# Kernel optimization log

Hardware: AMD Instinct MI355X
Metric: run time of the kernel (lower is better)

Reference implementation:

```python
import jax, jax.numpy as jnp
import numpy as np

B, S, D = 32, 1024, 1024
H = 16            # attention heads
T = 8             # num_tasks (probe tokens)
E = 8             # num_experts
K = 2             # top_k
HID = 4 * D       # expert hidden dim
EPS = 1e-5


def setup_inputs() -> dict:
    key = jax.random.key(0)
    ks = jax.random.split(key, 12)
    sd = 1.0 / np.sqrt(D)
    inp = {
        "x": jax.random.normal(ks[0], (B, S, D), jnp.float32),
        "probe": jax.random.normal(ks[1], (1, T, D), jnp.float32) * 0.02,
        "in_proj_w": jax.random.normal(ks[2], (3 * D, D), jnp.float32) * sd,
        "in_proj_b": jnp.zeros((3 * D,), jnp.float32),
        "out_proj_w": jax.random.normal(ks[3], (D, D), jnp.float32) * sd,
        "out_proj_b": jnp.zeros((D,), jnp.float32),
        "ln_gamma": jnp.ones((D,), jnp.float32),
        "ln_beta": jnp.zeros((D,), jnp.float32),
        "gate_w": jax.random.normal(ks[4], (T, D, E), jnp.float32) * sd,  # per-task gate (task-aware)
        "w1": jax.random.normal(ks[5], (E, D, HID), jnp.float32) * sd,
        "b1": jnp.zeros((E, HID), jnp.float32),
        "w2": jax.random.normal(ks[6], (E, HID, D), jnp.float32) / np.sqrt(HID),
        "b2": jnp.zeros((E, D), jnp.float32),
    }
    return inp


def reference(x, probe, in_proj_w, in_proj_b, out_proj_w, out_proj_b,
              ln_gamma, ln_beta, gate_w, w1, b1, w2, b2):
    b, s, d = x.shape
    t = probe.shape[1]
    dh = d // H
    # --- multihead cross attention: query = probe, key/value = x ---
    wq, wk, wv = in_proj_w[:d], in_proj_w[d:2 * d], in_proj_w[2 * d:]
    bq, bk, bv = in_proj_b[:d], in_proj_b[d:2 * d], in_proj_b[2 * d:]
    q = jnp.broadcast_to(probe, (b, t, d)) @ wq.T + bq           # [B,T,D]
    k = x @ wk.T + bk                                            # [B,S,D]
    v = x @ wv.T + bv
    q = q.reshape(b, t, H, dh).transpose(0, 2, 1, 3)             # bhtd
    k = k.reshape(b, s, H, dh).transpose(0, 2, 1, 3)             # bhsd
    v = v.reshape(b, s, H, dh).transpose(0, 2, 1, 3)
    scores = jnp.einsum('bhtd,bhsd->bhts', q, k) / np.sqrt(dh)
    attn = jax.nn.softmax(scores, axis=-1)                       # [B,H,T,S]
    ctx = jnp.einsum('bhts,bhsd->bhtd', attn, v)
    ctx = ctx.transpose(0, 2, 1, 3).reshape(b, t, d)
    attn_out = ctx @ out_proj_w.T + out_proj_b                   # [B,T,D]
    attn_weights = attn.mean(axis=1)                             # torch avg over heads
    # --- layernorm ---
    mu = attn_out.mean(-1, keepdims=True)
    var = attn_out.var(-1, keepdims=True)
    y = (attn_out - mu) * jax.lax.rsqrt(var + EPS) * ln_gamma + ln_beta
    # --- task-aware MoE: per-task gate, top-k routing ---
    logits = jnp.einsum('btd,tde->bte', y, gate_w)               # [B,T,E]
    probs = jax.nn.softmax(logits, axis=-1)
    tok = y.reshape(b * t, d)
    p = probs.reshape(b * t, E)
    topv, topi = jax.lax.top_k(p, K)                             # [N,K]
    wgt = topv / topv.sum(-1, keepdims=True)
    gates = jnp.zeros((b * t, E), y.dtype).at[jnp.arange(b * t)[:, None], topi].set(wgt)
    # all experts on all tokens (N=B*T is small); grouped GEMM form
    h = jax.nn.gelu(jnp.einsum('nd,edh->enh', tok, w1) + b1[:, None, :], approximate=False)
    eo = jnp.einsum('enh,ehd->end', h, w2) + b2[:, None, :]      # [E,N,D]
    moe_out = jnp.einsum('ne,end->nd', gates, eo).reshape(b, t, d)
    # load-balancing aux loss
    dispatch = (jax.nn.one_hot(topi, E, dtype=y.dtype)).sum(1)   # [N,E] 0/1
    f = dispatch.mean(0)
    P = p.mean(0)
    moe_loss = E * jnp.sum(f * P)
    final = attn_out + moe_out
    return final, moe_loss, attn_weights
```

## Files before the change

kernel.cpp:

```cpp
#include <hip/hip_runtime.h>
#include <hip/hip_bf16.h>
#include <math.h>


using bf16x8  = __attribute__((ext_vector_type(8))) short;
using f32x4   = __attribute__((ext_vector_type(4))) float;
using short4v = __attribute__((ext_vector_type(4))) short;

__device__ inline short f2bf(float f) {
  unsigned u = __builtin_bit_cast(unsigned, f);
  u = (u + 0x7fffu + ((u >> 16) & 1u)) >> 16;
  return (short)u;
}
__device__ inline int bswz(int k, int n) {
  return (((k >> 3) ^ ((n >> 2) & 3)) << 3) | (k & 7);
}

#define LGKM0() asm volatile("s_waitcnt lgkmcnt(0)" ::: "memory")
#define RAWBAR() do { __builtin_amdgcn_s_barrier(); __builtin_amdgcn_sched_barrier(0); } while (0)

static constexpr long OFF_Q       = 0;
static constexpr long OFF_QWB     = 8192;
static constexpr long OFF_QB      = 73728;
static constexpr long OFF_PSUM    = 73856;
static constexpr long OFF_FCNT    = 73864;
static constexpr long OFF_GATES   = 73872;
static constexpr long OFF_CTX     = 75920;
static constexpr long OFF_ATTNOUT = 338064;
static constexpr long OFF_EOP     = 600208;
static constexpr long OFF_CTXP    = 8988816;
static constexpr long OFF_AOP     = 10037392;
static constexpr long OFF_SCORES  = 11085968;
static constexpr long OFF_AXP     = 15280272;
static constexpr long OFF_YB      = 23668880;
static constexpr long OFF_HB      = 23799952;

__global__ __launch_bounds__(256) void compute_q_k(const float* __restrict__ probe,
                                                   const float* __restrict__ in_w,
                                                   const float* __restrict__ in_b,
                                                   float* __restrict__ q) {
  int wid = threadIdx.x >> 6, lane = threadIdx.x & 63;
  int idx = blockIdx.x * 4 + wid;
  int t = idx >> 10, d = idx & 1023;
  const float* pr = probe + (long)t * 1024;
  const float* wr = in_w + (long)d * 1024;
  float s = 0.f;
  for (int k = lane * 4; k < 1024; k += 256) {
    float4 a = *(const float4*)&pr[k];
    float4 b = *(const float4*)&wr[k];
    s += a.x * b.x + a.y * b.y + a.z * b.z + a.w * b.w;
  }
  for (int o = 32; o; o >>= 1) s += __shfl_xor(s, o);
  if (!lane) q[idx] = s + in_b[d];
}

__global__ __launch_bounds__(256) void compute_qw_k(const float* __restrict__ q,
                                                    const float* __restrict__ in_w,
                                                    const float* __restrict__ in_b,
                                                    short* __restrict__ qwb,
                                                    float* __restrict__ qb) {
  const int h = blockIdx.y;
  const int tid = threadIdx.x;
  const int d = blockIdx.x * 256 + tid;
  __shared__ float qh[8][64];
  if (tid < 64) {
#pragma unroll
    for (int t = 0; t < 8; ++t) qh[t][tid] = q[t * 1024 + h * 64 + tid] * 0.125f;
  }
  __syncthreads();
  const float* wk = in_w + 1048576 + (long)h * 64 * 1024;
  float acc[8];
#pragma unroll
  for (int t = 0; t < 8; ++t) acc[t] = 0.f;
  for (int j = 0; j < 64; ++j) {
    float w = wk[(long)j * 1024 + d];
#pragma unroll
    for (int t = 0; t < 8; ++t) acc[t] += qh[t][j] * w;
  }
#pragma unroll
  for (int t = 0; t < 8; ++t) qwb[(long)(h * 8 + t) * 1024 + d] = f2bf(acc[t]);
  if (blockIdx.x == 0 && tid < 8) {
    float s = 0.f;
    for (int j = 0; j < 64; ++j) s += qh[tid][j] * in_b[1024 + h * 64 + j];
    qb[h * 8 + tid] = s;
  }
}

__global__ __launch_bounds__(512)
void gemm_sc(const short* __restrict__ qwb, const float* __restrict__ xp,
             float* __restrict__ scores) {
  const int b = blockIdx.z;
  const int n0 = blockIdx.x * 64;
  const float* B = xp + (long)b * 1048576;
  float* C = scores + (long)b * 131072;
  const int tid = threadIdx.x;
  __shared__ short As[128][40], Bs[64][40];

  f32x4 acc[2][2];
#pragma unroll
  for (int i = 0; i < 2; ++i)
#pragma unroll
    for (int j = 0; j < 2; ++j)
#pragma unroll
      for (int qq = 0; qq < 4; ++qq) acc[i][j][qq] = 0.f;

  const int wid = tid >> 6, lane = tid & 63;
  const int wm = wid & 3, wn = wid >> 2;
  const int r = lane & 15, kg = (lane >> 4) * 8;
  const int am = tid >> 2, ak8 = (tid & 3) * 8;
  const int bn = tid >> 3, bk4 = (tid & 7) * 4;

  bf16x8 ra;
  float4 rb;
  auto loadT = [&](int k0) {
    ra = *(const bf16x8*)&qwb[(long)am * 1024 + k0 + ak8];
    rb = *(const float4*)&B[(long)(n0 + bn) * 1024 + k0 + bk4];
  };
  auto storeT = [&]() {
    *(bf16x8*)&As[am][ak8] = ra;
    short4v s;
    s.x = f2bf(rb.x); s.y = f2bf(rb.y); s.z = f2bf(rb.z); s.w = f2bf(rb.w);
    *(short4v*)&Bs[bn][bk4] = s;
  };
  auto compute = [&]() {
    bf16x8 af[2], bf_[2];
#pragma unroll
    for (int i = 0; i < 2; ++i) af[i] = *(const bf16x8*)&As[wm * 32 + i * 16 + r][kg];
#pragma unroll
    for (int j = 0; j < 2; ++j) bf_[j] = *(const bf16x8*)&Bs[wn * 32 + j * 16 + r][kg];
#pragma unroll
    for (int i = 0; i < 2; ++i)
#pragma unroll
      for (int j = 0; j < 2; ++j)
        acc[i][j] = __builtin_amdgcn_mfma_f32_16x16x32_bf16(af[i], bf_[j], acc[i][j], 0, 0, 0);
  };

  constexpr int NTILES = 32;
  loadT(0);
  storeT();
  loadT(32);
  LGKM0(); RAWBAR();
  for (int t = 0; t < NTILES; ++t) {
    compute();
    if (t + 1 < NTILES) {
      LGKM0(); RAWBAR();
      storeT();
      if (t + 2 < NTILES) loadT((t + 2) * 32);
      LGKM0(); RAWBAR();
    }
  }

  const int q4 = (lane >> 4) * 4;
#pragma unroll
  for (int i = 0; i < 2; ++i)
#pragma unroll
    for (int j = 0; j < 2; ++j) {
      int gn = n0 + wn * 32 + j * 16 + r;
#pragma unroll
      for (int qq = 0; qq < 4; ++qq) {
        int m = wm * 32 + i * 16 + q4 + qq;
        C[(long)m * 1024 + gn] = acc[i][j][qq];
      }
    }
}

template<int WM, int WN, int KS, bool AKB, bool BTRANS, int APL, int EPI>
__global__ __launch_bounds__(WM * WN * 64)
void gemm_ss(const float* __restrict__ Ap, const float* __restrict__ Bp,
             const float* __restrict__ kbias, float* __restrict__ Cp,
             int lda, int ldb, int K,
             long zA, long zA2, long zB, long zC, long ZKC, int ldc) {
  constexpr int BM = WM * 64, BN = WN * 64, BK = 32, NT = WM * WN * 64, PK = 40;
  constexpr int LA = BM * BK / (NT * 4), LB = BN * BK / (NT * 4);
  constexpr int F4 = BN / 4;
  const int z = blockIdx.z, zo = z / KS, kc = z % KS;
  const float* A = Ap + zA * zo + (long)kc * K;
  const float* B = BTRANS ? (Bp + zB * zo + (long)kc * K * ldb)
                          : (Bp + zB * zo + (long)kc * K);
  const float* kb = kbias + (long)kc * K;
  float* C = Cp + zC * zo + ZKC * kc;
  const int tid = threadIdx.x;
  const int m0 = blockIdx.y * BM, n0 = blockIdx.x * BN;
  __shared__ short Ah[BM][PK], Al[BM][PK], Bh[BN][PK], Bl[BN][PK];

  f32x4 acc[4][4];
#pragma unroll
  for (int i = 0; i < 4; ++i)
#pragma unroll
    for (int j = 0; j < 4; ++j)
#pragma unroll
      for (int qq = 0; qq < 4; ++qq) acc[i][j][qq] = 0.f;

  const int wid = tid >> 6, lane = tid & 63;
  const int wm = wid % WM, wn = wid / WM;
  const int r = lane & 15, kg = (lane >> 4) * 8;

  float4 ra[LA], rb[LB];

  auto loadT = [&](int k0) {
#pragma unroll
    for (int i = 0; i < LA; ++i) {
      int f = tid + i * NT;
      int m = f >> 3, k4 = (f & 7) * 4;
      long ofs = (long)(m0 + m) * lda + k0 + k4;
      ra[i] = *(const float4*)&A[ofs];
#pragma unroll
      for (int p = 1; p < APL; ++p) {
        float4 v2 = *(const float4*)&A[ofs + zA2 * p];
        ra[i].x += v2.x; ra[i].y += v2.y; ra[i].z += v2.z; ra[i].w += v2.w;
      }
      if (AKB) {
        float4 kv = *(const float4*)&kb[k0 + k4];
        ra[i].x += kv.x; ra[i].y += kv.y; ra[i].z += kv.z; ra[i].w += kv.w;
      }
    }
#pragma unroll
    for (int i = 0; i < LB; ++i) {
      int f = tid + i * NT;
      if (BTRANS) {
        int k = f / F4, n4 = (f % F4) * 4;
        rb[i] = *(const float4*)&B[(long)(k0 + k) * ldb + n0 + n4];
      } else {
        int n = f >> 3, k4 = (f & 7) * 4;
        rb[i] = *(const float4*)&B[(long)(n0 + n) * ldb + k0 + k4];
      }
    }
  };

  auto storeT = [&]() {
#pragma unroll
    for (int i = 0; i < LA; ++i) {
      int f = tid + i * NT;
      int m = f >> 3, k4 = (f & 7) * 4;
      short4v h, l;
      float vv[4] = {ra[i].x, ra[i].y, ra[i].z, ra[i].w};
#pragma unroll
      for (int j = 0; j < 4; ++j) {
        unsigned u = __builtin_bit_cast(unsigned, vv[j]);
        h[j] = (short)(u >> 16);
        l[j] = f2bf(vv[j] - __builtin_bit_cast(float, u & 0xFFFF0000u));
      }
      *(short4v*)&Ah[m][k4] = h;
      *(short4v*)&Al[m][k4] = l;
    }
#pragma unroll
    for (int i = 0; i < LB; ++i) {
      int f = tid + i * NT;
      float vv[4] = {rb[i].x, rb[i].y, rb[i].z, rb[i].w};
      if (BTRANS) {
        int k = f / F4, n4 = (f % F4) * 4;
        int col = bswz(k, n4);
#pragma unroll
        for (int j = 0; j < 4; ++j) {
          unsigned u = __builtin_bit_cast(unsigned, vv[j]);
          Bh[n4 + j][col] = (short)(u >> 16);
          Bl[n4 + j][col] = f2bf(vv[j] - __builtin_bit_cast(float, u & 0xFFFF0000u));
        }
      } else {
        int n = f >> 3, k4 = (f & 7) * 4;
        short4v h, l;
#pragma unroll
        for (int j = 0; j < 4; ++j) {
          unsigned u = __builtin_bit_cast(unsigned, vv[j]);
          h[j] = (short)(u >> 16);
          l[j] = f2bf(vv[j] - __builtin_bit_cast(float, u & 0xFFFF0000u));
        }
        *(short4v*)&Bh[n][k4] = h;
        *(short4v*)&Bl[n][k4] = l;
      }
    }
  };

  auto compute = [&]() {
    bf16x8 ah[4], al[4], bh[4], bl[4];
#pragma unroll
    for (int i = 0; i < 4; ++i) {
      ah[i] = *(const bf16x8*)&Ah[wm * 64 + i * 16 + r][kg];
      al[i] = *(const bf16x8*)&Al[wm * 64 + i * 16 + r][kg];
    }
#pragma unroll
    for (int j = 0; j < 4; ++j) {
      int brow = wn * 64 + j * 16 + r;
      int bcol = BTRANS ? bswz(kg, brow) : kg;
      bh[j] = *(const bf16x8*)&Bh[brow][bcol];
      bl[j] = *(const bf16x8*)&Bl[brow][bcol];
    }
#pragma unroll
    for (int i = 0; i < 4; ++i)
#pragma unroll
      for (int j = 0; j < 4; ++j) {
        acc[i][j] = __builtin_amdgcn_mfma_f32_16x16x32_bf16(ah[i], bh[j], acc[i][j], 0, 0, 0);
        acc[i][j] = __builtin_amdgcn_mfma_f32_16x16x32_bf16(ah[i], bl[j], acc[i][j], 0, 0, 0);
        acc[i][j] = __builtin_amdgcn_mfma_f32_16x16x32_bf16(al[i], bh[j], acc[i][j], 0, 0, 0);
      }
  };

  const int NTILES = K / BK;
  loadT(0);
  storeT();
  if (NTILES > 1) loadT(BK);
  LGKM0(); RAWBAR();
  for (int t = 0; t < NTILES; ++t) {
    compute();
    if (t + 1 < NTILES) {
      LGKM0(); RAWBAR();
      storeT();
      if (t + 2 < NTILES) loadT((t + 2) * BK);
      LGKM0(); RAWBAR();
    }
  }

  const int q4 = (lane >> 4) * 4;
#pragma unroll
  for (int i = 0; i < 4; ++i) {
    int gmb = m0 + wm * 64 + i * 16 + q4;
#pragma unroll
    for (int j = 0; j < 4; ++j) {
      int gn = n0 + wn * 64 + j * 16 + r;
#pragma unroll
      for (int qq = 0; qq < 4; ++qq) {
        float v = acc[i][j][qq];
        int m = gmb + qq;
        if constexpr (EPI == 0) {
          C[(long)m * ldc + gn] = v;
        } else {
          C[(long)(m >> 3) * 262144 + (long)(m & 7) * 1024 + gn] = v;
        }
      }
    }
  }
}

template<int KS, int EPI>
__global__ __launch_bounds__(128)
void gemm_bw(const short* __restrict__ Ap, const float* __restrict__ Bp,
             const float* __restrict__ biasp, void* __restrict__ Cp,
             int lda, int ldb, int K, long zA, long zB, long zBias, long zC, long ZKC, int ldc) {
  constexpr int BM = 128, BN = 64, BK = 64, NT = 128, PK = 72;
  constexpr int LA = BM * BK / (NT * 8);
  constexpr int LB = BN * BK / (NT * 4);
  constexpr int F4 = BN / 4;
  const int z = blockIdx.z, zo = z / KS, kc = z % KS;
  const short* A = Ap + zA * zo + (long)kc * K;
  const float* B = Bp + zB * zo + (long)kc * K * ldb;
  const float* bias = biasp + zBias * zo;
  const int tid = threadIdx.x;
  const int m0 = blockIdx.y * BM, n0 = blockIdx.x * BN;
  __shared__ short As[BM][PK], Bs[BN][PK];

  f32x4 acc[4][4];
#pragma unroll
  for (int i = 0; i < 4; ++i)
#pragma unroll
    for (int j = 0; j < 4; ++j)
#pragma unroll
      for (int qq = 0; qq < 4; ++qq) acc[i][j][qq] = 0.f;

  const int wid = tid >> 6, lane = tid & 63;
  const int wm = wid;
  const int r = lane & 15, kg = (lane >> 4) * 8;

  bf16x8 ra[LA];
  float4 rb[LB];

  auto loadT = [&](int k0) {
#pragma unroll
    for (int i = 0; i < LA; ++i) {
      int f = tid + i * NT;
      int m = f >> 3, k8 = (f & 7) * 8;
      ra[i] = *(const bf16x8*)&A[(long)(m0 + m) * lda + k0 + k8];
    }
#pragma unroll
    for (int i = 0; i < LB; ++i) {
      int f = tid + i * NT;
      int k = f / F4, n4 = (f % F4) * 4;
      rb[i] = *(const float4*)&B[(long)(k0 + k) * ldb + n0 + n4];
    }
  };

  auto storeT = [&]() {
#pragma unroll
    for (int i = 0; i < LA; ++i) {
      int f = tid + i * NT;
      int m = f >> 3, k8 = (f & 7) * 8;
      *(bf16x8*)&As[m][k8] = ra[i];
    }
#pragma unroll
    for (int i = 0; i < LB; ++i) {
      int f = tid + i * NT;
      int k = f / F4, n4 = (f % F4) * 4;
      int col = bswz(k, n4);
      Bs[n4 + 0][col] = f2bf(rb[i].x);
      Bs[n4 + 1][col] = f2bf(rb[i].y);
      Bs[n4 + 2][col] = f2bf(rb[i].z);
      Bs[n4 + 3][col] = f2bf(rb[i].w);
    }
  };

  auto compute = [&]() {
#pragma unroll
    for (int kk = 0; kk < 2; ++kk) {
      bf16x8 af[4], bfr[4];
#pragma unroll
      for (int i = 0; i < 4; ++i)
        af[i] = *(const bf16x8*)&As[wm * 64 + i * 16 + r][kk * 32 + kg];
#pragma unroll
      for (int j = 0; j < 4; ++j) {
        int brow = j * 16 + r;
        bfr[j] = *(const bf16x8*)&Bs[brow][bswz(kk * 32 + kg, brow)];
      }
#pragma unroll
      for (int i = 0; i < 4; ++i)
#pragma unroll
        for (int j = 0; j < 4; ++j)
          acc[i][j] = __builtin_amdgcn_mfma_f32_16x16x32_bf16(af[i], bfr[j], acc[i][j], 0, 0, 0);
    }
  };

  const int NTILES = K / BK;
  loadT(0);
  storeT();
  if (NTILES > 1) loadT(BK);
  LGKM0(); RAWBAR();
  for (int t = 0; t < NTILES; ++t) {
    compute();
    if (t + 1 < NTILES) {
      LGKM0(); RAWBAR();
      storeT();
      if (t + 2 < NTILES) loadT((t + 2) * BK);
      LGKM0(); RAWBAR();
    }
  }

  const int q4 = (lane >> 4) * 4;
#pragma unroll
  for (int i = 0; i < 4; ++i) {
    int gmb = m0 + wm * 64 + i * 16 + q4;
#pragma unroll
    for (int j = 0; j < 4; ++j) {
      int gn = n0 + j * 16 + r;
#pragma unroll
      for (int qq = 0; qq < 4; ++qq) {
        float v = acc[i][j][qq];
        int m = gmb + qq;
        if constexpr (EPI == 2) {
          float u = v + bias[gn];
          u = 0.5f * u * (1.0f + erff(u * 0.70710678118654752f));
          ((short*)Cp + zC * zo)[(long)m * ldc + gn] = f2bf(u);
        } else {
          ((float*)Cp + zC * zo + ZKC * kc)[(long)m * ldc + gn] = v;
        }
      }
    }
  }
}

__global__ __launch_bounds__(256) void reduce4_k(const float* __restrict__ p,
                                                 float* __restrict__ out) {
  int i = (blockIdx.x * 256 + threadIdx.x) * 4;
  float4 a = *(const float4*)&p[i];
  float4 b = *(const float4*)&p[i + 262144];
  float4 c = *(const float4*)&p[i + 524288];
  float4 d = *(const float4*)&p[i + 786432];
  float4 o;
  o.x = a.x + b.x + c.x + d.x;
  o.y = a.y + b.y + c.y + d.y;
  o.z = a.z + b.z + c.z + d.z;
  o.w = a.w + b.w + c.w + d.w;
  *(float4*)&out[i] = o;
}

__global__ __launch_bounds__(256) void softmax_k(float* __restrict__ scores,
                                                 const float* __restrict__ qb) {
  long row = blockIdx.x;
  float bias = qb[(int)(row & 127)];
  float* p = scores + row * 1024;
  int tid = threadIdx.x;
  int wid = tid >> 6, lane = tid & 63;
  float v[4];
  float mx = -1e30f;
#pragma unroll
  for (int i = 0; i < 4; ++i) {
    v[i] = p[tid + i * 256] + bias;
    mx = fmaxf(mx, v[i]);
  }
  for (int o = 32; o; o >>= 1) mx = fmaxf(mx, __shfl_xor(mx, o));
  __shared__ float sm[4];
  __shared__ float ss[4];
  if (!lane) sm[wid] = mx;
  __syncthreads();
  mx = fmaxf(fmaxf(sm[0], sm[1]), fmaxf(sm[2], sm[3]));
  float s = 0.f;
#pragma unroll
  for (int i = 0; i < 4; ++i) { v[i] = expf(v[i] - mx); s += v[i]; }
  for (int o = 32; o; o >>= 1) s += __shfl_xor(s, o);
  if (!lane) ss[wid] = s;
  __syncthreads();
  s = ss[0] + ss[1] + ss[2] + ss[3];
  float inv = 1.0f / s;
#pragma unroll
  for (int i = 0; i < 4; ++i) p[tid + i * 256] = v[i] * inv;
}

__global__ __launch_bounds__(256) void attnw_k(const float* __restrict__ attn,
                                               float* __restrict__ outw) {
  int idx = blockIdx.x * 256 + threadIdx.x;
  int b = idx >> 13;
  int r = idx & 8191;
  int t = r >> 10, s = r & 1023;
  const float* p = attn + (long)b * 131072 + (long)t * 1024 + s;
  float acc = 0.f;
#pragma unroll
  for (int h = 0; h < 16; ++h) acc += p[(long)h * 8192];
  outw[idx] = acc * (1.0f / 16.0f);
}

__global__ __launch_bounds__(256) void ln_gate_k(const float* __restrict__ aop,
                                                 const float* __restrict__ out_b,
                                                 const float* __restrict__ gamma,
                                                 const float* __restrict__ beta,
                                                 const float* __restrict__ gate_w,
                                                 float* __restrict__ attn_out,
                                                 short* __restrict__ yb,
                                                 float* __restrict__ gates,
                                                 float* __restrict__ Psum,
                                                 float* __restrict__ fcnt) {
  int row = blockIdx.x;
  int t = row & 7;
  int tid = threadIdx.x;
  int wid = tid >> 6, lane = tid & 63;
  const float* xr = aop + (long)row * 1024;
  float vals[4];
  float s = 0.f, sq = 0.f;
#pragma unroll
  for (int i = 0; i < 4; ++i) {
    int d = tid + i * 256;
    float v = xr[d] + xr[d + 262144] + xr[d + 524288] + xr[d + 786432] + out_b[d];
    attn_out[(long)row * 1024 + d] = v;
    vals[i] = v;
    s += v;
    sq += v * v;
  }
  for (int o = 32; o; o >>= 1) { s += __shfl_xor(s, o); sq += __shfl_xor(sq, o); }
  __shared__ float rs[4], rss[4];
  if (!lane) { rs[wid] = s; rss[wid] = sq; }
  __syncthreads();
  s = rs[0] + rs[1] + rs[2] + rs[3];
  sq = rss[0] + rss[1] + rss[2] + rss[3];
  float mu = s * (1.0f / 1024.0f);
  float var = sq * (1.0f / 1024.0f) - mu * mu;
  float rstd = rsqrtf(var + 1e-5f);
  __shared__ float yrow[1024];
#pragma unroll
  for (int i = 0; i < 4; ++i) {
    int d = tid + i * 256;
    float yv = (vals[i] - mu) * rstd * gamma[d] + beta[d];
    yb[(long)row * 1024 + d] = f2bf(yv);
    yrow[d] = yv;
  }
  __syncthreads();
  int e = tid & 7;
  int g = tid >> 3;
  float acc = 0.f;
  const float* gw = gate_w + (long)t * 8192;
  for (int d = g; d < 1024; d += 32) acc += yrow[d] * gw[d * 8 + e];
  __shared__ float part[256];
  __shared__ float lsh[8];
  part[tid] = acc;
  __syncthreads();
  if (tid < 8) {
    float l = 0.f;
    for (int gg = 0; gg < 32; ++gg) l += part[gg * 8 + tid];
    lsh[tid] = l;
  }
  __syncthreads();
  if (tid == 0) {
    float p[8];
    float mx = -1e30f;
    for (int k = 0; k < 8; ++k) mx = fmaxf(mx, lsh[k]);
    float sum = 0.f;
    for (int k = 0; k < 8; ++k) { p[k] = expf(lsh[k] - mx); sum += p[k]; }
    float inv = 1.0f / sum;
    for (int k = 0; k < 8; ++k) p[k] *= inv;
    int i0 = 0;
    for (int k = 1; k < 8; ++k) if (p[k] > p[i0]) i0 = k;
    int i1 = -1;
    for (int k = 0; k < 8; ++k) if (k != i0 && (i1 < 0 || p[k] > p[i1])) i1 = k;
    float tot = p[i0] + p[i1];
    for (int k = 0; k < 8; ++k)
      gates[(long)row * 8 + k] = (k == i0) ? p[i0] / tot : (k == i1) ? p[i1] / tot : 0.f;
    for (int k = 0; k < 8; ++k) atomicAdd(&Psum[k], p[k]);
    atomicAdd(&fcnt[i0], 1.0f);
    atomicAdd(&fcnt[i1], 1.0f);
  }
}

__global__ __launch_bounds__(256) void combine_k(const float* __restrict__ attn_out,
                                                 const float* __restrict__ eop,
                                                 const float* __restrict__ b2,
                                                 const float* __restrict__ gates,
                                                 float* __restrict__ outp) {
  int idx = blockIdx.x * 256 + threadIdx.x;
  int n = idx >> 10, d = idx & 1023;
  float v = attn_out[idx];
  const float* g = gates + (long)n * 8;
#pragma unroll
  for (int e = 0; e < 8; ++e) {
    float ge = g[e];
    if (ge != 0.f) {
      long base = (long)e * 262144 + idx;
      float s = eop[base] + eop[base + 2097152] + eop[base + 4194304] + eop[base + 6291456];
      v += ge * (s + b2[e * 1024 + d]);
    }
  }
  outp[idx] = v;
}

__global__ void loss_k(const float* __restrict__ Psum, const float* __restrict__ fcnt,
                       float* __restrict__ out) {
  if (threadIdx.x == 0) {
    float l = 0.f;
    for (int e = 0; e < 8; ++e) l += (fcnt[e] * (1.0f / 256.0f)) * (Psum[e] * (1.0f / 256.0f));
    out[0] = 8.0f * l;
  }
}

extern "C" void kernel_launch(void* const* d_in, const int* in_sizes, int n_in,
                              void* d_out, int out_size, void* d_ws, size_t ws_size,
                              hipStream_t stream) {
  const float* x      = (const float*)d_in[0];
  const float* probe  = (const float*)d_in[1];
  const float* in_w   = (const float*)d_in[2];
  const float* in_b   = (const float*)d_in[3];
  const float* out_w  = (const float*)d_in[4];
  const float* out_b  = (const float*)d_in[5];
  const float* gamma  = (const float*)d_in[6];
  const float* beta   = (const float*)d_in[7];
  const float* gate_w = (const float*)d_in[8];
  const float* w1     = (const float*)d_in[9];
  const float* b1     = (const float*)d_in[10];
  const float* w2     = (const float*)d_in[11];
  const float* b2     = (const float*)d_in[12];

  float* ws = (float*)d_ws;
  float* q        = ws + OFF_Q;
  short* qwb      = (short*)(ws + OFF_QWB);
  float* qb       = ws + OFF_QB;
  float* Psum     = ws + OFF_PSUM;
  float* fcnt     = ws + OFF_FCNT;
  float* gates    = ws + OFF_GATES;
  float* ctx      = ws + OFF_CTX;
  float* attn_out = ws + OFF_ATTNOUT;
  float* eop      = ws + OFF_EOP;
  float* ctxp     = ws + OFF_CTXP;
  float* aop      = ws + OFF_AOP;
  float* scores   = ws + OFF_SCORES;
  float* axp      = ws + OFF_AXP;
  short* yb       = (short*)(ws + OFF_YB);
  short* hb       = (short*)(ws + OFF_HB);

  float* out_final = (float*)d_out;
  float* out_loss  = out_final + 262144;
  float* out_attnw = out_loss + 1;

  hipMemsetAsync(ws + OFF_PSUM, 0, 16 * sizeof(float), stream);

  compute_q_k<<<2048, 256, 0, stream>>>(probe, in_w, in_b, q);
  compute_qw_k<<<dim3(4, 16, 1), 256, 0, stream>>>(q, in_w, in_b, qwb, qb);

  gemm_sc<<<dim3(16, 1, 32), 512, 0, stream>>>(qwb, x, scores);

  softmax_k<<<4096, 256, 0, stream>>>(scores, qb);
  attnw_k<<<1024, 256, 0, stream>>>(scores, out_attnw);

  gemm_ss<2, 2, 2, false, true, 1, 4><<<dim3(8, 1, 64), 256, 0, stream>>>(
      scores, x, qb , axp, 1024, 1024, 512,
      131072L, 0L, 1048576L, 8192L, 4194304L, 1024);

  gemm_ss<1, 1, 4, false, false, 2, 0><<<dim3(1, 4, 64), 64, 0, stream>>>(
      axp, in_w + 2097152, qb , ctxp, 1024, 1024, 256,
      262144L, 4194304L, 65536L, 64L, 262144L, 1024);
  reduce4_k<<<256, 256, 0, stream>>>(ctxp, ctx);

  gemm_ss<1, 1, 4, true, false, 1, 0><<<dim3(16, 4, 4), 64, 0, stream>>>(
      ctx, out_w, in_b + 2048, aop, 1024, 1024, 256,
      0L, 0L, 0L, 0L, 262144L, 1024);

  ln_gate_k<<<256, 256, 0, stream>>>(aop, out_b, gamma, beta, gate_w, attn_out,
                                     yb, gates, Psum, fcnt);

  gemm_bw<1, 2><<<dim3(64, 2, 8), 128, 0, stream>>>(
      yb, w1, b1, hb, 1024, 4096, 1024, 0L, 4194304L, 4096L, 1048576L, 0L, 4096);

  gemm_bw<4, 5><<<dim3(16, 2, 32), 128, 0, stream>>>(
      hb, w2, b2 , eop, 4096, 1024, 1024, 1048576L, 4194304L, 0L, 262144L, 2097152L, 1024);

  combine_k<<<1024, 256, 0, stream>>>(attn_out, eop, b2, gates, out_final);
  loss_k<<<1, 64, 0, stream>>>(Psum, fcnt, out_loss);
}
```

Baseline: 352.8 us.

## Cover all 256 MoE rows per block and transpose B tiles in registers

The expert GEMM kernel now uses 256-thread blocks whose tile spans all 256 token rows (BM=256). Each weight tile is therefore loaded and converted once per block instead of twice, which halves the fp32 weight traffic for the two expert GEMMs. Both the split-precision GEMM and the expert GEMM now load a 4x4 block of B per thread and transpose it in registers, so LDS writes are 4-wide short vectors rather than scalar shorts. The costs are half as many blocks in the grid, and the expert kernel now assumes M is exactly 256.

Result: faster. 328.5 us (-6.9%).

```diff
diff --git a/kernel.cpp b/kernel.cpp
--- a/kernel.cpp
+++ b/kernel.cpp
@@ -11,6 +11,9 @@
   unsigned u = __builtin_bit_cast(unsigned, f);
   u = (u + 0x7fffu + ((u >> 16) & 1u)) >> 16;
   return (short)u;
+}
+__device__ inline float f4get(const float4& v, int j) {
+  return j == 0 ? v.x : j == 1 ? v.y : j == 2 ? v.z : v.w;
 }
 __device__ inline int bswz(int k, int n) {
   return (((k >> 3) ^ ((n >> 2) & 3)) << 3) | (k & 7);
@@ -173,6 +176,7 @@
   constexpr int BM = WM * 64, BN = WN * 64, BK = 32, NT = WM * WN * 64, PK = 40;
   constexpr int LA = BM * BK / (NT * 4), LB = BN * BK / (NT * 4);
   constexpr int F4 = BN / 4;
+  constexpr int SLB = LB / 4;
   const int z = blockIdx.z, zo = z / KS, kc = z % KS;
   const float* A = Ap + zA * zo + (long)kc * K;
   const float* B = BTRANS ? (Bp + zB * zo + (long)kc * K * ldb)
@@ -214,13 +218,19 @@
         ra[i].x += kv.x; ra[i].y += kv.y; ra[i].z += kv.z; ra[i].w += kv.w;
       }
     }
-#pragma unroll
-    for (int i = 0; i < LB; ++i) {
-      int f = tid + i * NT;
-      if (BTRANS) {
-        int k = f / F4, n4 = (f % F4) * 4;
-        rb[i] = *(const float4*)&B[(long)(k0 + k) * ldb + n0 + n4];
-      } else {
+    if (BTRANS) {
+#pragma unroll
+      for (int s = 0; s < SLB; ++s) {
+        int slot = tid + s * NT;
+        int n4 = (slot % F4) * 4, k4 = (slot / F4) * 4;
+#pragma unroll
+        for (int j = 0; j < 4; ++j)
+          rb[s * 4 + j] = *(const float4*)&B[(long)(k0 + k4 + j) * ldb + n0 + n4];
+      }
+    } else {
+#pragma unroll
+      for (int i = 0; i < LB; ++i) {
+        int f = tid + i * NT;
         int n = f >> 3, k4 = (f & 7) * 4;
         rb[i] = *(const float4*)&B[(long)(n0 + n) * ldb + k0 + k4];
       }
@@ -243,21 +253,32 @@
       *(short4v*)&Ah[m][k4] = h;
       *(short4v*)&Al[m][k4] = l;
     }
-#pragma unroll
-    for (int i = 0; i < LB; ++i) {
-      int f = tid + i * NT;
-      float vv[4] = {rb[i].x, rb[i].y, rb[i].z, rb[i].w};
-      if (BTRANS) {
-        int k = f / F4, n4 = (f % F4) * 4;
-        int col = bswz(k, n4);
-#pragma unroll
-        for (int j = 0; j < 4; ++j) {
-          unsigned u = __builtin_bit_cast(unsigned, vv[j]);
-          Bh[n4 + j][col] = (short)(u >> 16);
-          Bl[n4 + j][col] = f2bf(vv[j] - __builtin_bit_cast(float, u & 0xFFFF0000u));
+    if (BTRANS) {
+#pragma unroll
+      for (int s = 0; s < SLB; ++s) {
+        int slot = tid + s * NT;
+        int n4 = (slot % F4) * 4, k4 = (slot / F4) * 4;
+        int col = bswz(k4, n4);
+#pragma unroll
+        for (int j2 = 0; j2 < 4; ++j2) {
+          short4v hh, ll;
+#pragma unroll
+          for (int jr = 0; jr < 4; ++jr) {
+            float v = f4get(rb[s * 4 + jr], j2);
+            unsigned u = __builtin_bit_cast(unsigned, v);
+            hh[jr] = (short)(u >> 16);
+            ll[jr] = f2bf(v - __builtin_bit_cast(float, u & 0xFFFF0000u));
+          }
+          *(short4v*)&Bh[n4 + j2][col] = hh;
+          *(short4v*)&Bl[n4 + j2][col] = ll;
         }
-      } else {
+      }
+    } else {
+#pragma unroll
+      for (int i = 0; i < LB; ++i) {
+        int f = tid + i * NT;
         int n = f >> 3, k4 = (f & 7) * 4;
+        float vv[4] = {rb[i].x, rb[i].y, rb[i].z, rb[i].w};
         short4v h, l;
 #pragma unroll
         for (int j = 0; j < 4; ++j) {
@@ -332,20 +353,19 @@
 }
 
 template<int KS, int EPI>
-__global__ __launch_bounds__(128)
+__global__ __launch_bounds__(256)
 void gemm_bw(const short* __restrict__ Ap, const float* __restrict__ Bp,
              const float* __restrict__ biasp, void* __restrict__ Cp,
              int lda, int ldb, int K, long zA, long zB, long zBias, long zC, long ZKC, int ldc) {
-  constexpr int BM = 128, BN = 64, BK = 64, NT = 128, PK = 72;
+  constexpr int BM = 256, BN = 64, BK = 64, NT = 256, PK = 72;
   constexpr int LA = BM * BK / (NT * 8);
-  constexpr int LB = BN * BK / (NT * 4);
   constexpr int F4 = BN / 4;
   const int z = blockIdx.z, zo = z / KS, kc = z % KS;
   const short* A = Ap + zA * zo + (long)kc * K;
   const float* B = Bp + zB * zo + (long)kc * K * ldb;
   const float* bias = biasp + zBias * zo;
   const int tid = threadIdx.x;
-  const int m0 = blockIdx.y * BM, n0 = blockIdx.x * BN;
+  const int n0 = blockIdx.x * BN;
   __shared__ short As[BM][PK], Bs[BN][PK];
 
   f32x4 acc[4][4];
@@ -359,23 +379,22 @@
   const int wid = tid >> 6, lane = tid & 63;
   const int wm = wid;
   const int r = lane & 15, kg = (lane >> 4) * 8;
+  const int sn4 = (tid & 15) * 4, sk4 = (tid >> 4) * 4;
+  const int scol = bswz(sk4, sn4);
 
   bf16x8 ra[LA];
-  float4 rb[LB];
+  float4 rb[4];
 
   auto loadT = [&](int k0) {
 #pragma unroll
     for (int i = 0; i < LA; ++i) {
       int f = tid + i * NT;
       int m = f >> 3, k8 = (f & 7) * 8;
-      ra[i] = *(const bf16x8*)&A[(long)(m0 + m) * lda + k0 + k8];
-    }
-#pragma unroll
-    for (int i = 0; i < LB; ++i) {
-      int f = tid + i * NT;
-      int k = f / F4, n4 = (f % F4) * 4;
-      rb[i] = *(const float4*)&B[(long)(k0 + k) * ldb + n0 + n4];
-    }
+      ra[i] = *(const bf16x8*)&A[(long)m * lda + k0 + k8];
+    }
+#pragma unroll
+    for (int j = 0; j < 4; ++j)
+      rb[j] = *(const float4*)&B[(long)(k0 + sk4 + j) * ldb + n0 + sn4];
   };
 
   auto storeT = [&]() {
@@ -386,14 +405,11 @@
       *(bf16x8*)&As[m][k8] = ra[i];
     }
 #pragma unroll
-    for (int i = 0; i < LB; ++i) {
-      int f = tid + i * NT;
-      int k = f / F4, n4 = (f % F4) * 4;
-      int col = bswz(k, n4);
-      Bs[n4 + 0][col] = f2bf(rb[i].x);
-      Bs[n4 + 1][col] = f2bf(rb[i].y);
-      Bs[n4 + 2][col] = f2bf(rb[i].z);
-      Bs[n4 + 3][col] = f2bf(rb[i].w);
+    for (int j2 = 0; j2 < 4; ++j2) {
+      short4v s;
+#pragma unroll
+      for (int jr = 0; jr < 4; ++jr) s[jr] = f2bf(f4get(rb[jr], j2));
+      *(short4v*)&Bs[sn4 + j2][scol] = s;
     }
   };
 
@@ -435,7 +451,7 @@
   const int q4 = (lane >> 4) * 4;
 #pragma unroll
   for (int i = 0; i < 4; ++i) {
-    int gmb = m0 + wm * 64 + i * 16 + q4;
+    int gmb = wm * 64 + i * 16 + q4;
 #pragma unroll
     for (int j = 0; j < 4; ++j) {
       int gn = n0 + j * 16 + r;
@@ -689,10 +705,10 @@
   ln_gate_k<<<256, 256, 0, stream>>>(aop, out_b, gamma, beta, gate_w, attn_out,
                                      yb, gates, Psum, fcnt);
 
-  gemm_bw<1, 2><<<dim3(64, 2, 8), 128, 0, stream>>>(
+  gemm_bw<1, 2><<<dim3(64, 1, 8), 256, 0, stream>>>(
       yb, w1, b1, hb, 1024, 4096, 1024, 0L, 4194304L, 4096L, 1048576L, 0L, 4096);
 
-  gemm_bw<4, 5><<<dim3(16, 2, 32), 128, 0, stream>>>(
+  gemm_bw<4, 5><<<dim3(16, 1, 32), 256, 0, stream>>>(
       hb, w2, b2 , eop, 4096, 1024, 1024, 1048576L, 4194304L, 0L, 262144L, 2097152L, 1024);
 
   combine_k<<<1024, 256, 0, stream>>>(attn_out, eop, b2, gates, out_final);
```
